# Kernel tuning notes

Measured on AMD Instinct MI355X. Metric: run time of the kernel, lower is better.

## Reference

```python
import jax, jax.numpy as jnp
import numpy as np

B, C, H, W = 2, 256, 256, 256
HEADS = 4
WSZ = 8
SR = 8
FILTER_RATE = 0.3


def setup_inputs() -> dict:
    key = jax.random.key(0)
    ks = jax.random.split(key, 8)
    return {
        "feature_map": jax.random.normal(ks[0], (B, C, H, W), jnp.float32),
        "uncertain_map": jax.random.uniform(ks[1], (B, H, W), jnp.float32),
        "sr_w": jax.random.normal(ks[2], (C, 1, SR, SR), jnp.float32) * np.sqrt(2.0 / (SR * SR)),
        "sr_b": jnp.zeros((C,), jnp.float32),
        "ln_g": jnp.ones((C,), jnp.float32),
        "ln_b": jnp.zeros((C,), jnp.float32),
        "wq_l": jax.random.normal(ks[3], (C, C), jnp.float32) * 0.02,
        "wkv_l": jax.random.normal(ks[4], (C, 2 * C), jnp.float32) * 0.02,
        "wq_g": jax.random.normal(ks[5], (C, C), jnp.float32) * 0.02,
        "wkv_g": jax.random.normal(ks[6], (C, 2 * C), jnp.float32) * 0.02,
        "wp": jax.random.normal(ks[7], (C, C), jnp.float32) * 0.02,
        "bp": jnp.zeros((C,), jnp.float32),
    }


def _layernorm(x, g, b, eps=1e-5):
    mu = x.mean(-1, keepdims=True)
    var = ((x - mu) ** 2).mean(-1, keepdims=True)
    return (x - mu) * jax.lax.rsqrt(var + eps) * g + b


def _mhsa(q, k, v, scale):
    # q,k,v: [..., heads, L, Ch]
    attn = jax.nn.softmax(jnp.einsum('...hqc,...hkc->...hqk', q, k) * scale, axis=-1)
    return jnp.einsum('...hqk,...hkc->...hqc', attn, v)


def reference(feature_map, uncertain_map, sr_w, sr_b, ln_g, ln_b,
              wq_l, wkv_l, wq_g, wkv_g, wp, bp):
    Bx, Cx, Hx, Wx = feature_map.shape
    Ch = Cx // HEADS
    scale = Ch ** -0.5
    nH, nW = Hx // WSZ, Wx // WSZ
    nWin = nH * nW
    winsz = WSZ * WSZ
    H1, W1 = Hx // SR, Wx // SR
    hw1 = H1 * W1
    nWF = int(nWin * FILTER_RATE)

    # --- windowize ---
    win_x = (feature_map.transpose(0, 2, 3, 1)
             .reshape(Bx, nH, WSZ, nW, WSZ, Cx)
             .transpose(0, 1, 3, 2, 4, 5)
             .reshape(Bx * nWin, winsz, Cx))
    win_unc = (uncertain_map.reshape(Bx, nH, WSZ, nW, WSZ)
               .transpose(0, 1, 3, 2, 4)
               .reshape(Bx, nWin, winsz))

    # --- top-k window selection ---
    win_score = win_unc.mean(-1)                        # [B, nWin]
    _, idx = jax.lax.top_k(win_score, nWF)              # [B, nWF]
    idx = (idx + jnp.arange(Bx)[:, None] * nWin).reshape(Bx * nWF)
    wf = win_x[idx]                                     # [B*nWF, winsz, C]

    # --- local window self-attention ---
    q = (wf @ wq_l).reshape(Bx * nWF, winsz, HEADS, Ch).transpose(0, 2, 1, 3)
    kv = (wf @ wkv_l).reshape(Bx * nWF, winsz, 2, HEADS, Ch)
    k = kv[:, :, 0].transpose(0, 2, 1, 3)
    v = kv[:, :, 1].transpose(0, 2, 1, 3)
    o = _mhsa(q, k, v, scale).transpose(0, 2, 1, 3).reshape(Bx * nWF, winsz, Cx)
    wf = wf + o

    # --- global branch: depthwise sr conv -> LN -> GELU ---
    g = jax.lax.conv_general_dilated(
        feature_map, sr_w, window_strides=(SR, SR), padding='VALID',
        feature_group_count=Cx,
        dimension_numbers=('NCHW', 'OIHW', 'NCHW')) + sr_b[None, :, None, None]
    g = g.reshape(Bx, Cx, hw1).transpose(0, 2, 1)       # [B, hw1, C]
    g = jax.nn.gelu(_layernorm(g, ln_g, ln_b), approximate=False)

    # --- global cross-attention (filtered windows attend to sr tokens) ---
    q = (wf.reshape(Bx, nWF * winsz, Cx) @ wq_g).reshape(Bx, nWF * winsz, HEADS, Ch).transpose(0, 2, 1, 3)
    kv = (g @ wkv_g).reshape(Bx, hw1, 2, HEADS, Ch)
    k = kv[:, :, 0].transpose(0, 2, 1, 3)
    v = kv[:, :, 1].transpose(0, 2, 1, 3)
    o = _mhsa(q, k, v, scale).transpose(0, 2, 1, 3).reshape(Bx * nWF, winsz, Cx)
    wf = wf + o

    # --- project and scatter-add back ---
    wf = wf @ wp + bp
    win_x = win_x.at[idx].add(wf)
    out = (win_x.reshape(Bx, nH, nW, WSZ, WSZ, Cx)
           .transpose(0, 5, 1, 3, 2, 4)
           .reshape(Bx, Cx, Hx, Wx))
    return out
```

## Files before the change

kernel.cpp:

```cpp
#include <hip/hip_runtime.h>
#include <math.h>

#define NWF    307
#define NWTOT  614
#define MROWS  39296

typedef float f32x4 __attribute__((ext_vector_type(4)));
typedef short s16x8 __attribute__((ext_vector_type(8)));

__device__ __forceinline__ short f2bf(float f) {
  unsigned int u = __builtin_bit_cast(unsigned int, f);
  u += 0x7fffu + ((u >> 16) & 1u);
  return (short)(u >> 16);
}

__device__ __forceinline__ unsigned int pk2bf(float lo, float hi) {
  return (unsigned int)(unsigned short)f2bf(lo) |
         ((unsigned int)(unsigned short)f2bf(hi) << 16);
}

__device__ __forceinline__ f32x4 mfma16(s16x8 a, s16x8 b, f32x4 c) {
  return __builtin_amdgcn_mfma_f32_16x16x32_bf16(a, b, c, 0, 0, 0);
}

__global__ __launch_bounds__(64) void score_k(const float* __restrict__ unc,
                                              float* __restrict__ scores) {
  int blk = blockIdx.x;
  int b = blk >> 10, t = blk & 1023;
  int ty = t >> 5, tx = t & 31;
  int lane = threadIdx.x;
  float v = unc[(size_t)b * 65536 + (size_t)(ty * 8 + (lane >> 3)) * 256 + tx * 8 + (lane & 7)];
  for (int m = 32; m; m >>= 1) v += __shfl_xor(v, m);
  if (lane == 0) scores[blk] = v * (1.0f / 64.0f);
}

__global__ __launch_bounds__(1024) void topk_k(const float* __restrict__ scores,
                                               int* __restrict__ selidx) {
  __shared__ float sc[1024];
  int b = blockIdx.x, t = threadIdx.x;
  float s = scores[b * 1024 + t];
  sc[t] = s;
  __syncthreads();
  int rank = 0;
  for (int j = 0; j < 1024; ++j) {
    float o = sc[j];
    rank += (o > s) || (o == s && j < t);
  }
  if (rank < NWF) selidx[b * NWF + rank] = t;
}

__global__ __launch_bounds__(256) void gather_k(const float* __restrict__ fm,
                                                const int* __restrict__ selidx,
                                                float* __restrict__ wf) {
  __shared__ float tile[64][33];
  int slot = blockIdx.x;
  int b = slot >= NWF;
  int w = selidx[slot];
  int y0 = (w >> 5) * 8, x0 = (w & 31) * 8;
  int tid = threadIdx.x;
  int j = tid & 7, i = (tid >> 3) & 7, c4 = tid >> 6;
  int cc2 = tid & 31, t4 = tid >> 5;
  for (int c0 = 0; c0 < 256; c0 += 32) {
    for (int cs = 0; cs < 8; ++cs) {
      int c = c0 + cs * 4 + c4;
      tile[i * 8 + j][cs * 4 + c4] =
          fm[((size_t)(b * 256 + c) * 256 + y0 + i) * 256 + x0 + j];
    }
    __syncthreads();
    for (int ts = 0; ts < 8; ++ts) {
      int tok = ts * 8 + t4;
      wf[(size_t)(slot * 64 + tok) * 256 + c0 + cc2] = tile[tok][cc2];
    }
    __syncthreads();
  }
}

__global__ __launch_bounds__(256) void convcopy_k(const float* __restrict__ fm,
                                                  const float* __restrict__ srw,
                                                  const float* __restrict__ srb,
                                                  const float* __restrict__ lng,
                                                  const float* __restrict__ lnb,
                                                  float* __restrict__ g,
                                                  float* __restrict__ out) {
  int blk = blockIdx.x;
  int b = blk >> 8, rr = blk & 255, ty = rr >> 3, txg = rr & 7;
  int c = threadIdx.x;
  int lane = c & 63, wv = c >> 6;
  size_t base = ((size_t)(b * 256 + c) * 256 + ty * 8) * 256 + txg * 32;
  const float* fp = fm + base;
  float* op = out + base;
  const float* wp = srw + c * 64;
  float acc[4] = {0.f, 0.f, 0.f, 0.f};
#pragma unroll
  for (int i = 0; i < 8; ++i) {
    f32x4 r[8];
#pragma unroll
    for (int u = 0; u < 8; ++u) r[u] = *(const f32x4*)(fp + (size_t)i * 256 + u * 4);
#pragma unroll
    for (int u = 0; u < 8; ++u) *(f32x4*)(op + (size_t)i * 256 + u * 4) = r[u];
    f32x4 w0 = *(const f32x4*)(wp + i * 8);
    f32x4 w1 = *(const f32x4*)(wp + i * 8 + 4);
#pragma unroll
    for (int t = 0; t < 4; ++t) {
      f32x4 ra = r[2 * t], rb = r[2 * t + 1];
      acc[t] += ra[0] * w0[0] + ra[1] * w0[1] + ra[2] * w0[2] + ra[3] * w0[3]
              + rb[0] * w1[0] + rb[1] * w1[1] + rb[2] * w1[2] + rb[3] * w1[3];
    }
  }
  float sb = srb[c];
#pragma unroll
  for (int t = 0; t < 4; ++t) acc[t] += sb;
  __shared__ float red[4][8];
#pragma unroll
  for (int t = 0; t < 4; ++t) {
    float s = acc[t], q = acc[t] * acc[t];
    for (int m = 32; m; m >>= 1) { s += __shfl_xor(s, m); q += __shfl_xor(q, m); }
    if (lane == 0) { red[t][wv] = s; red[t][4 + wv] = q; }
  }
  __syncthreads();
  float gc = lng[c], bc = lnb[c];
#pragma unroll
  for (int t = 0; t < 4; ++t) {
    float sum = red[t][0] + red[t][1] + red[t][2] + red[t][3];
    float sq  = red[t][4] + red[t][5] + red[t][6] + red[t][7];
    float mu  = sum * (1.f / 256.f);
    float var = sq * (1.f / 256.f) - mu * mu;
    float xn = (acc[t] - mu) * rsqrtf(var + 1e-5f);
    float y = xn * gc + bc;
    float ge = 0.5f * y * (1.f + erff(y * 0.70710678118654752f));
    g[(size_t)(b * 1024 + ty * 32 + txg * 4 + t) * 256 + c] = ge;
  }
}

__global__ __launch_bounds__(256) void wtrans_k(const float* __restrict__ W,
                                                short* __restrict__ Wt, int N) {
  int n = blockIdx.x, k = threadIdx.x;
  Wt[(size_t)n * 256 + k] = f2bf(W[(size_t)k * N + n]);
}

template <int EPI>
__global__ __launch_bounds__(256) void gemm_k(const float* __restrict__ X,
                                              const short* __restrict__ Wt,
                                              const float* __restrict__ bias,
                                              short* __restrict__ outb,
                                              short* __restrict__ outvT,
                                              float* __restrict__ outf,
                                              int kvshift, float scale) {
  const int lane = threadIdx.x & 63;
  const int wv = threadIdx.x >> 6;
  const int l16 = lane & 15, quad = lane >> 4;
  const int row0 = blockIdx.x * 64 + wv * 16;
  const int col0 = blockIdx.y * 128;
  f32x4 acc[8];
#pragma unroll
  for (int i = 0; i < 8; ++i) { acc[i][0] = 0.f; acc[i][1] = 0.f; acc[i][2] = 0.f; acc[i][3] = 0.f; }
  const float* xrow = X + (size_t)(row0 + l16) * 256 + quad * 8;
  const short* wbase = Wt + (size_t)(col0 + l16) * 256 + quad * 8;
#pragma unroll
  for (int ks = 0; ks < 8; ++ks) {
    f32x4 xa = *(const f32x4*)(xrow + ks * 32);
    f32x4 xb = *(const f32x4*)(xrow + ks * 32 + 4);
    s16x8 a;
    a[0] = f2bf(xa[0]); a[1] = f2bf(xa[1]); a[2] = f2bf(xa[2]); a[3] = f2bf(xa[3]);
    a[4] = f2bf(xb[0]); a[5] = f2bf(xb[1]); a[6] = f2bf(xb[2]); a[7] = f2bf(xb[3]);
#pragma unroll
    for (int nt = 0; nt < 8; ++nt) {
      s16x8 b = *(const s16x8*)(wbase + (size_t)nt * 16 * 256 + ks * 32);
      acc[nt] = mfma16(a, b, acc[nt]);
    }
  }
#pragma unroll
  for (int nt = 0; nt < 8; ++nt) {
#pragma unroll
    for (int r = 0; r < 4; ++r) {
      int col = col0 + nt * 16 + l16;
      int row = row0 + quad * 4 + r;
      float v = acc[nt][r];
      if (EPI == 0) {
        outb[(size_t)row * 256 + col] = f2bf(v * scale);
      } else if (EPI == 1) {
        if (col < 256) {
          outb[(size_t)row * 256 + col] = f2bf(v);
        } else {
          int c2 = col - 256, hh = c2 >> 6, ch = c2 & 63;
          int grp = row >> kvshift, tok = row & ((1 << kvshift) - 1);
          outvT[((size_t)((grp * 4 + hh) * 64 + ch) << kvshift) + tok] = f2bf(v);
        }
      } else {
        outf[(size_t)row * 256 + col] = v + bias[col];
      }
    }
  }
}

__global__ __launch_bounds__(256, 2) void attn_k(const short* __restrict__ qbuf,
                                                 const short* __restrict__ kbuf,
                                                 const short* __restrict__ vT,
                                                 float* __restrict__ wf, int kvlen) {
  __shared__ short Plds[4][16 * 64];
  const int w = threadIdx.x >> 6, lane = threadIdx.x & 63;
  const int l16 = lane & 15, quad = lane >> 4;
  const int win = blockIdx.x, h = w;
  const int qrow0 = win * 64;
  const int grp = (kvlen == 64) ? win : (win >= NWF ? 1 : 0);

  s16x8 aq[4][2];
#pragma unroll
  for (int qt = 0; qt < 4; ++qt)
#pragma unroll
    for (int ks = 0; ks < 2; ++ks)
      aq[qt][ks] = *(const s16x8*)(qbuf + (size_t)(qrow0 + qt * 16 + l16) * 256 + h * 64 + ks * 32 + quad * 8);

  f32x4 O[4][4];
  float m2[4], li[4];
#pragma unroll
  for (int qt = 0; qt < 4; ++qt) {
    m2[qt] = -1e30f; li[qt] = 0.f;
#pragma unroll
    for (int nt = 0; nt < 4; ++nt)
#pragma unroll
      for (int r = 0; r < 4; ++r) O[qt][nt][r] = 0.f;
  }

  const short* kp = kbuf + ((size_t)grp * kvlen + l16) * 256 + h * 64 + quad * 8;
  const short* vp = vT + ((size_t)((grp * 4 + h) * 64) + l16) * kvlen + quad * 8;
  char* Pw = (char*)&Plds[w][0] + l16 * 128;
  const int sw = (l16 & 7) << 4;
  const int ntile = kvlen >> 6;

  for (int t = 0; t < ntile; ++t) {
    s16x8 kr[2][4];
#pragma unroll
    for (int ks = 0; ks < 2; ++ks)
#pragma unroll
      for (int nt = 0; nt < 4; ++nt)
        kr[ks][nt] = *(const s16x8*)(kp + (size_t)nt * 16 * 256 + ks * 32);
    s16x8 vr[2][4];
#pragma unroll
    for (int ks2 = 0; ks2 < 2; ++ks2)
#pragma unroll
      for (int nt = 0; nt < 4; ++nt)
        vr[ks2][nt] = *(const s16x8*)(vp + (size_t)nt * 16 * kvlen + ks2 * 32);

#pragma unroll
    for (int qt = 0; qt < 4; ++qt) {
      f32x4 S[4];
#pragma unroll
      for (int nt = 0; nt < 4; ++nt)
#pragma unroll
        for (int r = 0; r < 4; ++r) S[nt][r] = 0.f;
#pragma unroll
      for (int ks = 0; ks < 2; ++ks)
#pragma unroll
        for (int nt = 0; nt < 4; ++nt)
          S[nt] = mfma16(kr[ks][nt], aq[qt][ks], S[nt]);
      float mx = S[0][0];
#pragma unroll
      for (int nt = 0; nt < 4; ++nt)
#pragma unroll
        for (int r = 0; r < 4; ++r) mx = fmaxf(mx, S[nt][r]);
      mx = fmaxf(mx, __shfl_xor(mx, 16));
      mx = fmaxf(mx, __shfl_xor(mx, 32));
      if (__any(mx > m2[qt] + 8.0f)) {
        float mn = fmaxf(m2[qt], mx);
        float al = __builtin_amdgcn_exp2f(m2[qt] - mn);
        m2[qt] = mn;
        li[qt] *= al;
        float alr[4];
#pragma unroll
        for (int r = 0; r < 4; ++r) alr[r] = __shfl(al, quad * 4 + r);
#pragma unroll
        for (int nt = 0; nt < 4; ++nt)
#pragma unroll
          for (int r = 0; r < 4; ++r) O[qt][nt][r] *= alr[r];
      }
      float rs = 0.f;
#pragma unroll
      for (int nt = 0; nt < 4; ++nt)
#pragma unroll
        for (int r = 0; r < 4; ++r) {
          float p = __builtin_amdgcn_exp2f(S[nt][r] - m2[qt]);
          S[nt][r] = p;
          rs += p;
        }
      li[qt] += rs;
#pragma unroll
      for (int nt = 0; nt < 4; ++nt) {
        uint2 pw;
        pw.x = pk2bf(S[nt][0], S[nt][1]);
        pw.y = pk2bf(S[nt][2], S[nt][3]);
        *(uint2*)(Pw + ((nt * 32 + quad * 8) ^ sw)) = pw;
      }
#pragma unroll
      for (int ks2 = 0; ks2 < 2; ++ks2) {
        s16x8 ap = *(const s16x8*)(Pw + ((ks2 * 64 + quad * 16) ^ sw));
#pragma unroll
        for (int nt = 0; nt < 4; ++nt)
          O[qt][nt] = mfma16(ap, vr[ks2][nt], O[qt][nt]);
      }
    }
    kp += 64 * 256;
    vp += 64;
  }

#pragma unroll
  for (int qt = 0; qt < 4; ++qt) {
    float l = li[qt];
    l += __shfl_xor(l, 16);
    l += __shfl_xor(l, 32);
    float inv = 1.f / l;
    float invr[4];
#pragma unroll
    for (int r = 0; r < 4; ++r) invr[r] = __shfl(inv, quad * 4 + r);
#pragma unroll
    for (int nt = 0; nt < 4; ++nt)
#pragma unroll
      for (int r = 0; r < 4; ++r) {
        size_t oi = (size_t)(qrow0 + qt * 16 + quad * 4 + r) * 256 + h * 64 + nt * 16 + l16;
        wf[oi] += O[qt][nt][r] * invr[r];
      }
  }
}

__global__ __launch_bounds__(256) void scatter_k(const float* __restrict__ proj,
                                                 const int* __restrict__ selidx,
                                                 float* __restrict__ out) {
  __shared__ float tile[64][33];
  int slot = blockIdx.x;
  int b = slot >= NWF;
  int w = selidx[slot];
  int y0 = (w >> 5) * 8, x0 = (w & 31) * 8;
  int tid = threadIdx.x;
  int cc2 = tid & 31, t4 = tid >> 5;
  int j = tid & 7, i = (tid >> 3) & 7, c4 = tid >> 6;
  for (int c0 = 0; c0 < 256; c0 += 32) {
    for (int ts = 0; ts < 8; ++ts) {
      int tok = ts * 8 + t4;
      tile[tok][cc2] = proj[(size_t)(slot * 64 + tok) * 256 + c0 + cc2];
    }
    __syncthreads();
    for (int cs = 0; cs < 8; ++cs) {
      int c = c0 + cs * 4 + c4;
      size_t oidx = ((size_t)(b * 256 + c) * 256 + y0 + i) * 256 + x0 + j;
      out[oidx] += tile[i * 8 + j][cs * 4 + c4];
    }
    __syncthreads();
  }
}

extern "C" void kernel_launch(void* const* d_in, const int* in_sizes, int n_in,
                              void* d_out, int out_size, void* d_ws, size_t ws_size,
                              hipStream_t stream) {
  const float* fm    = (const float*)d_in[0];
  const float* unc   = (const float*)d_in[1];
  const float* srw   = (const float*)d_in[2];
  const float* srb   = (const float*)d_in[3];
  const float* lng   = (const float*)d_in[4];
  const float* lnb   = (const float*)d_in[5];
  const float* wq_l  = (const float*)d_in[6];
  const float* wkv_l = (const float*)d_in[7];
  const float* wq_g  = (const float*)d_in[8];
  const float* wkv_g = (const float*)d_in[9];
  const float* wpm   = (const float*)d_in[10];
  const float* bp    = (const float*)d_in[11];
  float* out = (float*)d_out;

  char* ws = (char*)d_ws;
  size_t off = 0;
  auto alloc = [&](size_t bytes) -> char* {
    char* p = ws + off;
    off += (bytes + 255) & ~(size_t)255;
    return p;
  };
  float* wf     = (float*)alloc((size_t)MROWS * 256 * 4);
  short* qbuf   = (short*)alloc((size_t)MROWS * 256 * 2);
  short* kbufl  = (short*)alloc((size_t)MROWS * 256 * 2);
  short* vTl    = (short*)alloc((size_t)MROWS * 256 * 2);
  short* kbufg  = (short*)alloc((size_t)2048 * 256 * 2);
  short* vTg    = (short*)alloc((size_t)2048 * 256 * 2);
  float* g      = (float*)alloc((size_t)2048 * 256 * 4);
  float* scores = (float*)alloc(2048 * 4);
  int*   selidx = (int*)alloc(NWTOT * 4);
  short* wtql   = (short*)alloc(256 * 256 * 2);
  short* wtkvl  = (short*)alloc(512 * 256 * 2);
  short* wtqg   = (short*)alloc(256 * 256 * 2);
  short* wtkvg  = (short*)alloc(512 * 256 * 2);
  short* wtp    = (short*)alloc(256 * 256 * 2);
  float* proj   = (float*)qbuf;

  const float C1 = 0.125f * 1.4426950408889634f;

  wtrans_k<<<256, 256, 0, stream>>>(wq_l, wtql, 256);
  wtrans_k<<<512, 256, 0, stream>>>(wkv_l, wtkvl, 512);
  wtrans_k<<<256, 256, 0, stream>>>(wq_g, wtqg, 256);
  wtrans_k<<<512, 256, 0, stream>>>(wkv_g, wtkvg, 512);
  wtrans_k<<<256, 256, 0, stream>>>(wpm, wtp, 256);

  score_k<<<2048, 64, 0, stream>>>(unc, scores);
  topk_k<<<2, 1024, 0, stream>>>(scores, selidx);
  gather_k<<<NWTOT, 256, 0, stream>>>(fm, selidx, wf);

  convcopy_k<<<512, 256, 0, stream>>>(fm, srw, srb, lng, lnb, g, out);

  gemm_k<0><<<dim3(NWTOT, 2), 256, 0, stream>>>(wf, wtql, nullptr, qbuf, nullptr, nullptr, 0, C1);
  gemm_k<1><<<dim3(NWTOT, 4), 256, 0, stream>>>(wf, wtkvl, nullptr, kbufl, vTl, nullptr, 6, 1.0f);
  attn_k<<<NWTOT, 256, 0, stream>>>(qbuf, kbufl, vTl, wf, 64);

  gemm_k<0><<<dim3(NWTOT, 2), 256, 0, stream>>>(wf, wtqg, nullptr, qbuf, nullptr, nullptr, 0, C1);
  gemm_k<1><<<dim3(32, 4), 256, 0, stream>>>(g, wtkvg, nullptr, kbufg, vTg, nullptr, 10, 1.0f);
  attn_k<<<NWTOT, 256, 0, stream>>>(qbuf, kbufg, vTg, wf, 1024);

  gemm_k<2><<<dim3(NWTOT, 2), 256, 0, stream>>>(wf, wtp, bp, nullptr, nullptr, proj, 0, 1.0f);
  scatter_k<<<NWTOT, 256, 0, stream>>>(proj, selidx, out);
}
```

Measured before the change: 929.7 us.

## Split conv-copy into coalesced per-channel conv kernel plus separate LayerNorm-GELU kernel

The depthwise strided conv plus full feature-map copy is restructured so that each block handles one channel and one 8-row strip. Consecutive lanes now read contiguous 16-byte chunks instead of each thread striding across channels. The LayerNorm and GELU over channels move into a new kernel that reads an intermediate buffer. This adds an extra launch and an extra round trip of a 2 MB buffer, in exchange for far better coalescing and many more blocks on the bandwidth-bound copy of the 128 MB input.

```diff
diff --git a/kernel.cpp b/kernel.cpp
--- a/kernel.cpp
+++ b/kernel.cpp
@@ -78,42 +78,49 @@
 __global__ __launch_bounds__(256) void convcopy_k(const float* __restrict__ fm,
                                                   const float* __restrict__ srw,
                                                   const float* __restrict__ srb,
-                                                  const float* __restrict__ lng,
-                                                  const float* __restrict__ lnb,
-                                                  float* __restrict__ g,
+                                                  float* __restrict__ g0,
                                                   float* __restrict__ out) {
   int blk = blockIdx.x;
-  int b = blk >> 8, rr = blk & 255, ty = rr >> 3, txg = rr & 7;
+  int c = blk & 255, ty = (blk >> 8) & 31, b = blk >> 13;
+  int t = threadIdx.x;
+  int w = t >> 6, l = t & 63;
+  size_t base = ((size_t)(b * 256 + c) * 256 + ty * 8) * 256;
+  const float* wp = srw + c * 64;
+  int j0 = (l & 1) * 4;
+  float acc = 0.f;
+#pragma unroll
+  for (int it = 0; it < 2; ++it) {
+    int row = it * 4 + w;
+    size_t off = base + (size_t)row * 256 + l * 4;
+    f32x4 v = *(const f32x4*)(fm + off);
+    *(f32x4*)(out + off) = v;
+    f32x4 wv = *(const f32x4*)(wp + row * 8 + j0);
+    acc += v[0] * wv[0] + v[1] * wv[1] + v[2] * wv[2] + v[3] * wv[3];
+  }
+  acc += __shfl_xor(acc, 1);
+  __shared__ float red[32][5];
+  if ((l & 1) == 0) red[l >> 1][w] = acc;
+  __syncthreads();
+  if (t < 32) {
+    float s = red[t][0] + red[t][1] + red[t][2] + red[t][3] + srb[c];
+    g0[(size_t)(b * 1024 + ty * 32 + t) * 256 + c] = s;
+  }
+}
+
+__global__ __launch_bounds__(256) void lnact_k(const float* __restrict__ g0,
+                                               const float* __restrict__ lng,
+                                               const float* __restrict__ lnb,
+                                               float* __restrict__ g) {
+  int tok4 = blockIdx.x;
   int c = threadIdx.x;
   int lane = c & 63, wv = c >> 6;
-  size_t base = ((size_t)(b * 256 + c) * 256 + ty * 8) * 256 + txg * 32;
-  const float* fp = fm + base;
-  float* op = out + base;
-  const float* wp = srw + c * 64;
-  float acc[4] = {0.f, 0.f, 0.f, 0.f};
-#pragma unroll
-  for (int i = 0; i < 8; ++i) {
-    f32x4 r[8];
-#pragma unroll
-    for (int u = 0; u < 8; ++u) r[u] = *(const f32x4*)(fp + (size_t)i * 256 + u * 4);
-#pragma unroll
-    for (int u = 0; u < 8; ++u) *(f32x4*)(op + (size_t)i * 256 + u * 4) = r[u];
-    f32x4 w0 = *(const f32x4*)(wp + i * 8);
-    f32x4 w1 = *(const f32x4*)(wp + i * 8 + 4);
-#pragma unroll
-    for (int t = 0; t < 4; ++t) {
-      f32x4 ra = r[2 * t], rb = r[2 * t + 1];
-      acc[t] += ra[0] * w0[0] + ra[1] * w0[1] + ra[2] * w0[2] + ra[3] * w0[3]
-              + rb[0] * w1[0] + rb[1] * w1[1] + rb[2] * w1[2] + rb[3] * w1[3];
-    }
-  }
-  float sb = srb[c];
-#pragma unroll
-  for (int t = 0; t < 4; ++t) acc[t] += sb;
+  float x[4];
+#pragma unroll
+  for (int t = 0; t < 4; ++t) x[t] = g0[(size_t)(tok4 * 4 + t) * 256 + c];
   __shared__ float red[4][8];
 #pragma unroll
   for (int t = 0; t < 4; ++t) {
-    float s = acc[t], q = acc[t] * acc[t];
+    float s = x[t], q = x[t] * x[t];
     for (int m = 32; m; m >>= 1) { s += __shfl_xor(s, m); q += __shfl_xor(q, m); }
     if (lane == 0) { red[t][wv] = s; red[t][4 + wv] = q; }
   }
@@ -125,10 +132,9 @@
     float sq  = red[t][4] + red[t][5] + red[t][6] + red[t][7];
     float mu  = sum * (1.f / 256.f);
     float var = sq * (1.f / 256.f) - mu * mu;
-    float xn = (acc[t] - mu) * rsqrtf(var + 1e-5f);
+    float xn = (x[t] - mu) * rsqrtf(var + 1e-5f);
     float y = xn * gc + bc;
-    float ge = 0.5f * y * (1.f + erff(y * 0.70710678118654752f));
-    g[(size_t)(b * 1024 + ty * 32 + txg * 4 + t) * 256 + c] = ge;
+    g[(size_t)(tok4 * 4 + t) * 256 + c] = 0.5f * y * (1.f + erff(y * 0.70710678118654752f));
   }
 }
 
@@ -379,6 +385,7 @@
   short* kbufg  = (short*)alloc((size_t)2048 * 256 * 2);
   short* vTg    = (short*)alloc((size_t)2048 * 256 * 2);
   float* g      = (float*)alloc((size_t)2048 * 256 * 4);
+  float* g0     = (float*)alloc((size_t)2048 * 256 * 4);
   float* scores = (float*)alloc(2048 * 4);
   int*   selidx = (int*)alloc(NWTOT * 4);
   short* wtql   = (short*)alloc(256 * 256 * 2);
@@ -400,7 +407,8 @@
   topk_k<<<2, 1024, 0, stream>>>(scores, selidx);
   gather_k<<<NWTOT, 256, 0, stream>>>(fm, selidx, wf);
 
-  convcopy_k<<<512, 256, 0, stream>>>(fm, srw, srb, lng, lnb, g, out);
+  convcopy_k<<<16384, 256, 0, stream>>>(fm, srw, srb, g0, out);
+  lnact_k<<<512, 256, 0, stream>>>(g0, lng, lnb, g);
 
   gemm_k<0><<<dim3(NWTOT, 2), 256, 0, stream>>>(wf, wtql, nullptr, qbuf, nullptr, nullptr, 0, C1);
   gemm_k<1><<<dim3(NWTOT, 4), 256, 0, stream>>>(wf, wtkvl, nullptr, kbufl, vTl, nullptr, 6, 1.0f);
```

New measurement: 827.2 us. -11.0%, faster.
